# Kernel tuning notes

Hardware: AMD Instinct MI355X
Metric: run time of the kernel (lower is better)

## Reference

```python
import jax, jax.numpy as jnp
import numpy as np

B, S, D, H, L = 16, 1024, 128, 8, 3
DFF = 4 * D  # 512
DH = D // H  # 16
NUM_CLASSES = 6


def layernorm(x, g, b, eps):
    mu = jnp.mean(x, axis=-1, keepdims=True)
    var = jnp.mean(jnp.square(x - mu), axis=-1, keepdims=True)
    return g * (x - mu) / jnp.sqrt(var + eps) + b


def setup_inputs() -> dict:
    key = jax.random.key(0)
    ks = jax.random.split(key, 16)
    sc = 0.05
    inp = {
        'x': jax.random.normal(ks[0], (B, S, D), dtype=jnp.float32),
        'Wq': jax.random.normal(ks[1], (L, D, D), dtype=jnp.float32) * sc,
        'bq': jnp.zeros((L, D), dtype=jnp.float32),
        'Wk': jax.random.normal(ks[2], (L, D, D), dtype=jnp.float32) * sc,
        'bk': jnp.zeros((L, D), dtype=jnp.float32),
        'Wv': jax.random.normal(ks[3], (L, D, D), dtype=jnp.float32) * sc,
        'bv': jnp.zeros((L, D), dtype=jnp.float32),
        'ln1_g': jnp.ones((L, D), dtype=jnp.float32),
        'ln1_b': jnp.zeros((L, D), dtype=jnp.float32),
        'W1': jax.random.normal(ks[4], (L, D, DFF), dtype=jnp.float32) * sc,
        'b1': jnp.zeros((L, DFF), dtype=jnp.float32),
        'W2': jax.random.normal(ks[5], (L, DFF, D), dtype=jnp.float32) * sc,
        'b2': jnp.zeros((L, D), dtype=jnp.float32),
        'ln2_g': jnp.ones((L, D), dtype=jnp.float32),
        'ln2_b': jnp.zeros((L, D), dtype=jnp.float32),
        'Wout': jax.random.normal(ks[6], (D, NUM_CLASSES), dtype=jnp.float32) * sc,
        'bout': jnp.zeros((NUM_CLASSES,), dtype=jnp.float32),
    }
    return inp


def reference(x, Wq, bq, Wk, bk, Wv, bv, ln1_g, ln1_b, W1, b1, W2, b2, ln2_g, ln2_b, Wout, bout):
    scale = 1.0 / jnp.sqrt(jnp.float32(DH))
    for l in range(L):
        # Q/K/V projections with ReLU activation (as in source Dense(..., relu))
        q = jax.nn.relu(jnp.einsum('bsd,de->bse', x, Wq[l]) + bq[l])
        k = jax.nn.relu(jnp.einsum('bsd,de->bse', x, Wk[l]) + bk[l])
        v = jax.nn.relu(jnp.einsum('bsd,de->bse', x, Wv[l]) + bv[l])
        # split-heads (tf.split axis=-1 / concat axis=0 == reshape to heads)
        qh = q.reshape(B, S, H, DH)
        kh = k.reshape(B, S, H, DH)
        vh = v.reshape(B, S, H, DH)
        scores = jnp.einsum('bqhd,bkhd->bhqk', qh, kh) * scale  # [B,H,S,S]
        attn = jax.nn.softmax(scores, axis=-1)
        o = jnp.einsum('bhqk,bkhd->bqhd', attn, vh).reshape(B, S, D)
        x = layernorm(o + x, ln1_g[l], ln1_b[l], 1e-8)
        # pointwise FFN (Conv1D kernel_size=1 == dense over last dim)
        h = jax.nn.relu(jnp.einsum('bsd,df->bsf', x, W1[l]) + b1[l])
        f = jnp.einsum('bsf,fd->bsd', h, W2[l]) + b2[l]
        x = layernorm(f + x, ln2_g[l], ln2_b[l], 1e-6)
    return jnp.einsum('bsd,dc->bsc', x, Wout) + bout
```

## Files before the change

### kernel.cpp

```cpp
#include <hip/hip_runtime.h>
#include <math.h>

#define Bq 16
#define Sq 1024
#define Dq 128
#define Hq 8
#define DHq 16
#define DFFq 512
#define Lq 3
#define NCLS 6
#define NROWS (Bq * Sq)
#define NX ((size_t)NROWS * Dq)

#define QSCL 0.36067376022224085f

typedef __attribute__((ext_vector_type(8))) short    bf16x8;
typedef __attribute__((ext_vector_type(4))) float    f32x4;
typedef __attribute__((ext_vector_type(4))) _Float16 f16x4;
typedef __attribute__((ext_vector_type(8))) _Float16 f16x8;
typedef __attribute__((ext_vector_type(2))) _Float16 f16x2;

__device__ inline ushort f32_to_bf16(float f) {
    union { float f; unsigned u; } v; v.f = f;
    unsigned r = v.u + 0x7fffu + ((v.u >> 16) & 1u);
    return (ushort)(r >> 16);
}

__device__ __forceinline__ float exp2_raw(float x) {
    float r;
    asm("v_exp_f32 %0, %1" : "=v"(r) : "v"(x));
    return r;
}

__device__ __forceinline__ float rcp_fast(float x) {
    float r;
    asm("v_rcp_f32 %0, %1" : "=v"(r) : "v"(x));
    return r;
}

__device__ __forceinline__ f16x2 pkrtz(float a, float b) {
    return __builtin_bit_cast(f16x2, __builtin_amdgcn_cvt_pkrtz(a, b));
}

__global__ __launch_bounds__(256) void prep_kernel(
    const float* __restrict__ Wqp, const float* __restrict__ Wkp,
    const float* __restrict__ Wvp, const float* __restrict__ W1p,
    const float* __restrict__ W2p, const float* __restrict__ xp,
    ushort* __restrict__ wbf, ushort* __restrict__ xbf)
{
    const int gid = blockIdx.x * 256 + threadIdx.x;
    if (gid < 147456) {
        const int w   = gid / 49152;
        const int rem = gid - w * 49152;
        const int l   = rem >> 14;
        const int idx = rem & 16383;
        const int k   = idx >> 7;
        const int n   = idx & 127;
        const float* src = (w == 0) ? Wqp : (w == 1) ? Wkp : Wvp;
        const float scl = (w == 0) ? QSCL : 1.0f;
        wbf[(size_t)(w * 3 + l) * 16384 + n * 128 + k] =
            f32_to_bf16(src[(size_t)l * 16384 + k * 128 + n] * scl);
    } else if (gid < 344064) {
        const int g   = gid - 147456;
        const int l   = g >> 16;
        const int idx = g & 65535;
        const int k   = idx >> 9;
        const int n   = idx & 511;
        wbf[147456 + (size_t)l * 65536 + n * 128 + k] =
            f32_to_bf16(W1p[(size_t)l * 65536 + k * 512 + n]);
    } else if (gid < 540672) {
        const int g   = gid - 344064;
        const int l   = g >> 16;
        const int idx = g & 65535;
        const int k   = idx >> 7;
        const int n   = idx & 127;
        wbf[344064 + (size_t)l * 65536 + n * 512 + k] =
            f32_to_bf16(W2p[(size_t)l * 65536 + k * 128 + n]);
    } else {
        const int g = gid - 540672;
        xbf[g] = f32_to_bf16(xp[g]);
    }
}

__global__ __launch_bounds__(256) void gemm_qkv(
    const ushort* __restrict__ A,
    const ushort* __restrict__ wq, const ushort* __restrict__ wk,
    const ushort* __restrict__ wv,
    const float* __restrict__ bqp, const float* __restrict__ bkp,
    const float* __restrict__ bvp,
    _Float16* __restrict__ qo, _Float16* __restrict__ ko,
    _Float16* __restrict__ vo)
{
    __shared__ ushort As[64 * 40];
    __shared__ ushort Bs[128 * 40];

    const int sel  = blockIdx.y;
    const ushort* Bt   = (sel == 0) ? wq : (sel == 1) ? wk : wv;
    const float*  bias = (sel == 0) ? bqp : (sel == 1) ? bkp : bvp;
    const float   bscl = (sel == 0) ? QSCL : 1.0f;

    const int tid  = threadIdx.x;
    const int row0 = blockIdx.x * 64;
    const int wave = tid >> 6;
    const int lane = tid & 63;
    const int quad = lane >> 4;
    const int m16  = lane & 15;
    const int wm   = wave >> 1;
    const int wn   = wave & 1;

    const int sar = tid >> 2;
    const int sac = (tid & 3) * 8;

    f32x4 acc[2][4];
    #pragma unroll
    for (int i = 0; i < 2; ++i)
        #pragma unroll
        for (int j = 0; j < 4; ++j) acc[i][j] = (f32x4)0.f;

    const int r1 = tid >> 2, r2 = r1 + 64;

    bf16x8 av  = *(const bf16x8*)(A  + (size_t)(row0 + sar) * 128 + sac);
    bf16x8 bv1 = *(const bf16x8*)(Bt + (size_t)r1 * 128 + sac);
    bf16x8 bv2 = *(const bf16x8*)(Bt + (size_t)r2 * 128 + sac);

    for (int k0 = 0; k0 < 128; k0 += 32) {
        __syncthreads();
        *(bf16x8*)&As[sar * 40 + sac] = av;
        *(bf16x8*)&Bs[r1 * 40 + sac]  = bv1;
        *(bf16x8*)&Bs[r2 * 40 + sac]  = bv2;
        __syncthreads();

        if (k0 < 96) {
            av  = *(const bf16x8*)(A  + (size_t)(row0 + sar) * 128 + k0 + 32 + sac);
            bv1 = *(const bf16x8*)(Bt + (size_t)r1 * 128 + k0 + 32 + sac);
            bv2 = *(const bf16x8*)(Bt + (size_t)r2 * 128 + k0 + 32 + sac);
        }

        bf16x8 af[2], bf[4];
        #pragma unroll
        for (int i = 0; i < 2; ++i)
            af[i] = *(const bf16x8*)&As[(32 * wm + 16 * i + m16) * 40 + quad * 8];
        #pragma unroll
        for (int j = 0; j < 4; ++j)
            bf[j] = *(const bf16x8*)&Bs[(64 * wn + 16 * j + m16) * 40 + quad * 8];
        #pragma unroll
        for (int i = 0; i < 2; ++i)
            #pragma unroll
            for (int j = 0; j < 4; ++j)
                acc[i][j] = __builtin_amdgcn_mfma_f32_16x16x32_bf16(af[i], bf[j], acc[i][j], 0, 0, 0);
    }

    #pragma unroll
    for (int i = 0; i < 2; ++i) {
        #pragma unroll
        for (int j = 0; j < 4; ++j) {
            const int col = 64 * wn + 16 * j + m16;
            const float bb = bias[col] * bscl;
            const int hh = col >> 4, dh = col & 15;
            #pragma unroll
            for (int r = 0; r < 4; ++r) {
                float val = fmaxf(acc[i][j][r] + bb, 0.f);
                const int gr = row0 + 32 * wm + 16 * i + quad * 4 + r;
                const int b = gr >> 10, s = gr & 1023;
                if (sel == 2) {
                    vo[(((size_t)b * Hq + hh) * DHq + dh) * Sq + s] = (_Float16)val;
                } else {
                    _Float16* outp = (sel == 0) ? qo : ko;
                    outp[(((size_t)b * Hq + hh) * Sq + s) * DHq + dh] = (_Float16)val;
                }
            }
        }
    }
}

__global__ __launch_bounds__(256) void gemm_ffn_fused(
    const _Float16* __restrict__ o, const float* __restrict__ resid,
    const float* __restrict__ g1, const float* __restrict__ beta1,
    const ushort* __restrict__ W1t, const float* __restrict__ bias1,
    const ushort* __restrict__ W2t, const float* __restrict__ bias2,
    const float* __restrict__ g2, const float* __restrict__ beta2,
    float* __restrict__ xb,
    const ushort* __restrict__ wqn, const ushort* __restrict__ wkn,
    const ushort* __restrict__ wvn,
    const float* __restrict__ bqn, const float* __restrict__ bkn,
    const float* __restrict__ bvn,
    _Float16* __restrict__ qo, _Float16* __restrict__ ko,
    _Float16* __restrict__ vo, int do_next,
    const float* __restrict__ Wout, const float* __restrict__ bout,
    float* __restrict__ out, int last)
{
    __shared__ __align__(16) char smem[69120];
    ushort*    Af   = (ushort*)smem;
    ushort*    Hs   = (ushort*)(smem + 8704);
    ushort*    Bs   = (ushort*)(smem + 41984);
    float*     wo_s = (float*)(smem + 41984);
    _Float16*  vals = (_Float16*)(smem + 60416);
    float*     mus  = (float*)(smem + 68864);
    float*     rsds = (float*)(smem + 68992);

    const int tid  = threadIdx.x;
    const int row0 = blockIdx.x * 32;
    const int wave = tid >> 6;
    const int lane = tid & 63;
    const int quad = lane >> 4;
    const int m16  = lane & 15;
    const int wm   = wave >> 1;
    const int wn   = wave & 1;
    const int sac  = (tid & 3) * 8;
    const int r1   = tid >> 2, r2 = r1 + 64;

    const int ca = lane * 2;
    const float2 gg  = *(const float2*)(g1 + ca);
    const float2 bt1 = *(const float2*)(beta1 + ca);
    #pragma unroll 2
    for (int it = 0; it < 8; ++it) {
        const int rr = wave * 8 + it;
        const size_t base = (size_t)(row0 + rr) * Dq;
        const f16x2  ov = *(const f16x2*)(o + base + ca);
        const float2 rv = *(const float2*)(resid + base + ca);
        const float v0 = (float)ov[0] + rv.x;
        const float v1 = (float)ov[1] + rv.y;

        float s = v0 + v1;
        #pragma unroll
        for (int off = 32; off > 0; off >>= 1) s += __shfl_xor(s, off, 64);
        const float mu = s * (1.f / 128.f);
        const float d0 = v0 - mu, d1 = v1 - mu;
        float vs = d0 * d0 + d1 * d1;
        #pragma unroll
        for (int off = 32; off > 0; off >>= 1) vs += __shfl_xor(vs, off, 64);
        const float rstd = rsqrtf(vs * (1.f / 128.f) + 1e-8f);

        const float rv0 = gg.x * d0 * rstd + bt1.x;
        const float rv1 = gg.y * d1 * rstd + bt1.y;
        ushort2 ab; ab.x = f32_to_bf16(rv0); ab.y = f32_to_bf16(rv1);
        *(ushort2*)&Af[rr * 136 + ca] = ab;
        f16x2 vv; vv[0] = (_Float16)rv0; vv[1] = (_Float16)rv1;
        *(f16x2*)&vals[rr * 132 + ca] = vv;
    }

    f32x4 acc[4];
    #pragma unroll
    for (int j = 0; j < 4; ++j) acc[j] = (f32x4)0.f;

    bf16x8 w11 = *(const bf16x8*)(W1t + (size_t)r1 * 128 + sac);
    bf16x8 w12 = *(const bf16x8*)(W1t + (size_t)r1 * 128 + 32 + sac);
    bf16x8 w21 = *(const bf16x8*)(W1t + (size_t)r2 * 128 + sac);
    bf16x8 w22 = *(const bf16x8*)(W1t + (size_t)r2 * 128 + 32 + sac);

    for (int idx = 0; idx < 8; ++idx) {
        const int cc = idx >> 1;
        const int k0 = (idx & 1) * 64;

        __syncthreads();
        *(bf16x8*)&Bs[r1 * 72 + sac]      = w11;
        *(bf16x8*)&Bs[r1 * 72 + 32 + sac] = w12;
        *(bf16x8*)&Bs[r2 * 72 + sac]      = w21;
        *(bf16x8*)&Bs[r2 * 72 + 32 + sac] = w22;
        __syncthreads();

        if (idx < 7) {
            const int cc2 = (idx + 1) >> 1;
            const int k02 = ((idx + 1) & 1) * 64;
            w11 = *(const bf16x8*)(W1t + (size_t)(cc2 * 128 + r1) * 128 + k02 + sac);
            w12 = *(const bf16x8*)(W1t + (size_t)(cc2 * 128 + r1) * 128 + k02 + 32 + sac);
            w21 = *(const bf16x8*)(W1t + (size_t)(cc2 * 128 + r2) * 128 + k02 + sac);
            w22 = *(const bf16x8*)(W1t + (size_t)(cc2 * 128 + r2) * 128 + k02 + 32 + sac);
        }

        #pragma unroll
        for (int hh = 0; hh < 2; ++hh) {
            const int kk = k0 + hh * 32;
            const bf16x8 af = *(const bf16x8*)&Af[(16 * wm + m16) * 136 + kk + quad * 8];
            bf16x8 bf[4];
            #pragma unroll
            for (int j = 0; j < 4; ++j)
                bf[j] = *(const bf16x8*)&Bs[(64 * wn + 16 * j + m16) * 72 + hh * 32 + quad * 8];
            #pragma unroll
            for (int j = 0; j < 4; ++j)
                acc[j] = __builtin_amdgcn_mfma_f32_16x16x32_bf16(af, bf[j], acc[j], 0, 0, 0);
        }

        if (idx & 1) {
            #pragma unroll
            for (int j = 0; j < 4; ++j) {
                const int col = cc * 128 + 64 * wn + 16 * j + m16;
                const float bb = bias1[col];
                #pragma unroll
                for (int r = 0; r < 4; ++r) {
                    const int row = 16 * wm + quad * 4 + r;
                    Hs[row * 520 + col] = f32_to_bf16(fmaxf(acc[j][r] + bb, 0.f));
                }
                acc[j] = (f32x4)0.f;
            }
        }
    }

    f32x4 acc2[4];
    #pragma unroll
    for (int j = 0; j < 4; ++j) acc2[j] = (f32x4)0.f;

    w11 = *(const bf16x8*)(W2t + (size_t)r1 * DFFq + sac);
    w12 = *(const bf16x8*)(W2t + (size_t)r1 * DFFq + 32 + sac);
    w21 = *(const bf16x8*)(W2t + (size_t)r2 * DFFq + sac);
    w22 = *(const bf16x8*)(W2t + (size_t)r2 * DFFq + 32 + sac);

    for (int kc = 0; kc < 8; ++kc) {
        const int k0 = kc * 64;

        __syncthreads();
        *(bf16x8*)&Bs[r1 * 72 + sac]      = w11;
        *(bf16x8*)&Bs[r1 * 72 + 32 + sac] = w12;
        *(bf16x8*)&Bs[r2 * 72 + sac]      = w21;
        *(bf16x8*)&Bs[r2 * 72 + 32 + sac] = w22;
        __syncthreads();

        if (kc < 7) {
            const int k02 = (kc + 1) * 64;
            w11 = *(const bf16x8*)(W2t + (size_t)r1 * DFFq + k02 + sac);
            w12 = *(const bf16x8*)(W2t + (size_t)r1 * DFFq + k02 + 32 + sac);
            w21 = *(const bf16x8*)(W2t + (size_t)r2 * DFFq + k02 + sac);
            w22 = *(const bf16x8*)(W2t + (size_t)r2 * DFFq + k02 + 32 + sac);
        }

        #pragma unroll
        for (int hh = 0; hh < 2; ++hh) {
            const int kk = k0 + hh * 32;
            const bf16x8 af = *(const bf16x8*)&Hs[(16 * wm + m16) * 520 + kk + quad * 8];
            bf16x8 bf[4];
            #pragma unroll
            for (int j = 0; j < 4; ++j)
                bf[j] = *(const bf16x8*)&Bs[(64 * wn + 16 * j + m16) * 72 + hh * 32 + quad * 8];
            #pragma unroll
            for (int j = 0; j < 4; ++j)
                acc2[j] = __builtin_amdgcn_mfma_f32_16x16x32_bf16(af, bf[j], acc2[j], 0, 0, 0);
        }
    }

    __syncthreads();

    float vreg[4][4];
    #pragma unroll
    for (int j = 0; j < 4; ++j) {
        const int col = 64 * wn + 16 * j + m16;
        const float bb = bias2[col];
        #pragma unroll
        for (int r = 0; r < 4; ++r) {
            const int row = 16 * wm + quad * 4 + r;
            float v = acc2[j][r] + bb + (float)vals[row * 132 + col];
            vreg[j][r] = v;
            vals[row * 132 + col] = (_Float16)v;
        }
    }
    if (last) {
        #pragma unroll
        for (int i = 0; i < 3; ++i) wo_s[tid + i * 256] = Wout[tid + i * 256];
    }
    __syncthreads();

    {
        const int row = tid >> 3;
        const int c0  = (tid & 7) * 16;
        float s = 0.f, s2 = 0.f;
        #pragma unroll
        for (int u = 0; u < 4; ++u) {
            const f16x4 xv = *(const f16x4*)&vals[row * 132 + c0 + u * 4];
            #pragma unroll
            for (int e = 0; e < 4; ++e) {
                const float x = (float)xv[e];
                s += x; s2 = fmaf(x, x, s2);
            }
        }
        s  += __shfl_xor(s, 1, 64);  s  += __shfl_xor(s, 2, 64);  s  += __shfl_xor(s, 4, 64);
        s2 += __shfl_xor(s2, 1, 64); s2 += __shfl_xor(s2, 2, 64); s2 += __shfl_xor(s2, 4, 64);
        if ((tid & 7) == 0) {
            const float mu  = s * (1.f / 128.f);
            const float var = s2 * (1.f / 128.f) - mu * mu;
            mus[row]  = mu;
            rsds[row] = rsqrtf(var + 1e-6f);
        }
    }
    __syncthreads();

    if (!last) {
        #pragma unroll
        for (int j = 0; j < 4; ++j) {
            const int col = 64 * wn + 16 * j + m16;
            #pragma unroll
            for (int r = 0; r < 4; ++r) {
                const int row = 16 * wm + quad * 4 + r;
                const float rn = g2[col] * (vreg[j][r] - mus[row]) * rsds[row] + beta2[col];
                xb[(size_t)(row0 + row) * Dq + col] = rn;
                Af[row * 136 + col] = f32_to_bf16(rn);
            }
        }

        if (do_next) {
            bf16x8 q11 = *(const bf16x8*)(wqn + (size_t)r1 * 128 + sac);
            bf16x8 q12 = *(const bf16x8*)(wqn + (size_t)r1 * 128 + 32 + sac);
            bf16x8 q21 = *(const bf16x8*)(wqn + (size_t)r2 * 128 + sac);
            bf16x8 q22 = *(const bf16x8*)(wqn + (size_t)r2 * 128 + 32 + sac);

            f32x4 qacc[4];
            for (int st = 0; st < 6; ++st) {
                const int sel  = st >> 1;
                const int half = st & 1;
                if (half == 0) {
                    #pragma unroll
                    for (int j = 0; j < 4; ++j) qacc[j] = (f32x4)0.f;
                }

                __syncthreads();
                *(bf16x8*)&Bs[r1 * 72 + sac]      = q11;
                *(bf16x8*)&Bs[r1 * 72 + 32 + sac] = q12;
                *(bf16x8*)&Bs[r2 * 72 + sac]      = q21;
                *(bf16x8*)&Bs[r2 * 72 + 32 + sac] = q22;
                __syncthreads();

                if (st < 5) {
                    const int sel2 = (st + 1) >> 1;
                    const int k02  = ((st + 1) & 1) * 64;
                    const ushort* Bt2 = (sel2 == 0) ? wqn : (sel2 == 1) ? wkn : wvn;
                    q11 = *(const bf16x8*)(Bt2 + (size_t)r1 * 128 + k02 + sac);
                    q12 = *(const bf16x8*)(Bt2 + (size_t)r1 * 128 + k02 + 32 + sac);
                    q21 = *(const bf16x8*)(Bt2 + (size_t)r2 * 128 + k02 + sac);
                    q22 = *(const bf16x8*)(Bt2 + (size_t)r2 * 128 + k02 + 32 + sac);
                }

                const int k0 = half * 64;
                #pragma unroll
                for (int hh = 0; hh < 2; ++hh) {
                    const int kk = k0 + hh * 32;
                    const bf16x8 af = *(const bf16x8*)&Af[(16 * wm + m16) * 136 + kk + quad * 8];
                    bf16x8 bf[4];
                    #pragma unroll
                    for (int j = 0; j < 4; ++j)
                        bf[j] = *(const bf16x8*)&Bs[(64 * wn + 16 * j + m16) * 72 + hh * 32 + quad * 8];
                    #pragma unroll
                    for (int j = 0; j < 4; ++j)
                        qacc[j] = __builtin_amdgcn_mfma_f32_16x16x32_bf16(af, bf[j], qacc[j], 0, 0, 0);
                }

                if (half) {
                    const float* bias = (sel == 0) ? bqn : (sel == 1) ? bkn : bvn;
                    const float  bscl = (sel == 0) ? QSCL : 1.0f;
                    #pragma unroll
                    for (int j = 0; j < 4; ++j) {
                        const int col = 64 * wn + 16 * j + m16;
                        const float bb = bias[col] * bscl;
                        const int hh = col >> 4, dh = col & 15;
                        #pragma unroll
                        for (int r = 0; r < 4; ++r) {
                            float val = fmaxf(qacc[j][r] + bb, 0.f);
                            const int gr = row0 + 16 * wm + quad * 4 + r;
                            const int b = gr >> 10, s = gr & 1023;
                            if (sel == 2) {
                                vo[(((size_t)b * Hq + hh) * DHq + dh) * Sq + s] = (_Float16)val;
                            } else {
                                _Float16* outp = (sel == 0) ? qo : ko;
                                outp[(((size_t)b * Hq + hh) * Sq + s) * DHq + dh] = (_Float16)val;
                            }
                        }
                    }
                }
            }
        }
    } else {
        #pragma unroll
        for (int j = 0; j < 4; ++j) {
            const int col = 64 * wn + 16 * j + m16;
            #pragma unroll
            for (int r = 0; r < 4; ++r) {
                const int row = 16 * wm + quad * 4 + r;
                vals[row * 132 + col] =
                    (_Float16)(g2[col] * (vreg[j][r] - mus[row]) * rsds[row] + beta2[col]);
            }
        }
        __syncthreads();
        if (tid < 32 * NCLS) {
            const int row = tid / NCLS;
            const int c   = tid - row * NCLS;
            float a = bout[c];
            #pragma unroll 8
            for (int kk = 0; kk < Dq; ++kk)
                a = fmaf((float)vals[row * 132 + kk], wo_s[kk * NCLS + c], a);
            out[(size_t)(row0 + row) * NCLS + c] = a;
        }
    }
}

__global__ __launch_bounds__(256) void attn_mfma(
    const _Float16* __restrict__ q, const _Float16* __restrict__ k,
    const _Float16* __restrict__ vt, _Float16* __restrict__ o)
{
    __shared__ _Float16 Ks[256 * 20];
    __shared__ _Float16 Vs[16 * 264];

    const int bh   = blockIdx.x;
    const int qc   = blockIdx.y;
    const int b    = bh >> 3;
    const int h    = bh & 7;
    const int tid  = threadIdx.x;
    const int wave = tid >> 6;
    const int lane = tid & 63;
    const int quad = lane >> 4;
    const int m16  = lane & 15;
    const int q0   = qc * 128 + wave * 32;

    const f16x4 qf0 = *(const f16x4*)(q + (((size_t)bh * Sq) + q0 + m16) * DHq + quad * 4);
    const f16x4 qf1 = *(const f16x4*)(q + (((size_t)bh * Sq) + q0 + 16 + m16) * DHq + quad * 4);

    const _Float16* kg  = k  + (size_t)bh * Sq * DHq;
    const _Float16* vtg = vt + (size_t)bh * DHq * Sq;

    f32x4 oacc0 = (f32x4)0.f, oacc1 = (f32x4)0.f;
    f32x4 dacc0 = (f32x4)0.f, dacc1 = (f32x4)0.f;

    f16x4 onesf;
    onesf[0] = (_Float16)1.f; onesf[1] = (_Float16)1.f;
    onesf[2] = (_Float16)1.f; onesf[3] = (_Float16)1.f;

    const int krow = tid;
    const int vrow = tid >> 4;
    const int vcol = (tid & 15) * 16;

    f16x8 ka  = *(const f16x8*)(kg + (size_t)krow * DHq);
    f16x8 kb8 = *(const f16x8*)(kg + (size_t)krow * DHq + 8);
    f16x8 va  = *(const f16x8*)(vtg + (size_t)vrow * Sq + vcol);
    f16x8 vb  = *(const f16x8*)(vtg + (size_t)vrow * Sq + vcol + 8);

    for (int kb = 0; kb < 4; ++kb) {
        __syncthreads();
        *(f16x8*)&Ks[krow * 20 + 0] = ka;
        *(f16x8*)&Ks[krow * 20 + 8] = kb8;
        *(f16x8*)&Vs[vrow * 264 + vcol + 0] = va;
        *(f16x8*)&Vs[vrow * 264 + vcol + 8] = vb;
        __syncthreads();

        if (kb < 3) {
            const _Float16* kp = kg  + ((size_t)(kb + 1) * 256 + krow) * DHq;
            const _Float16* vp = vtg + (size_t)vrow * Sq + (kb + 1) * 256 + vcol;
            ka  = *(const f16x8*)(kp);
            kb8 = *(const f16x8*)(kp + 8);
            va  = *(const f16x8*)(vp);
            vb  = *(const f16x8*)(vp + 8);
        }

        __builtin_amdgcn_s_setprio(1);
        #pragma unroll 4
        for (int kt = 0; kt < 16; ++kt) {
            const f16x4 kf = *(const f16x4*)&Ks[(kt * 16 + m16) * 20 + quad * 4];
            const f16x4 vf = *(const f16x4*)&Vs[m16 * 264 + kt * 16 + quad * 4];

            f32x4 st0 = __builtin_amdgcn_mfma_f32_16x16x16f16(kf, qf0, (f32x4)0.f, 0, 0, 0);
            f32x4 st1 = __builtin_amdgcn_mfma_f32_16x16x16f16(kf, qf1, (f32x4)0.f, 0, 0, 0);

            const f16x2 a0 = pkrtz(exp2_raw(st0[0]), exp2_raw(st0[1]));
            const f16x2 a1 = pkrtz(exp2_raw(st0[2]), exp2_raw(st0[3]));
            const f16x2 b0 = pkrtz(exp2_raw(st1[0]), exp2_raw(st1[1]));
            const f16x2 b1 = pkrtz(exp2_raw(st1[2]), exp2_raw(st1[3]));

            const f16x4 pf0 = __builtin_shufflevector(a0, a1, 0, 1, 2, 3);
            const f16x4 pf1 = __builtin_shufflevector(b0, b1, 0, 1, 2, 3);

            oacc0 = __builtin_amdgcn_mfma_f32_16x16x16f16(pf0, vf, oacc0, 0, 0, 0);
            oacc1 = __builtin_amdgcn_mfma_f32_16x16x16f16(pf1, vf, oacc1, 0, 0, 0);
            dacc0 = __builtin_amdgcn_mfma_f32_16x16x16f16(pf0, onesf, dacc0, 0, 0, 0);
            dacc1 = __builtin_amdgcn_mfma_f32_16x16x16f16(pf1, onesf, dacc1, 0, 0, 0);
        }
        __builtin_amdgcn_s_setprio(0);
    }

    #pragma unroll
    for (int r = 0; r < 4; ++r) {
        const float i0 = rcp_fast(dacc0[r]);
        const float i1 = rcp_fast(dacc1[r]);
        o[((size_t)b * Sq + q0 + quad * 4 + r) * Dq + h * DHq + m16]      = (_Float16)(oacc0[r] * i0);
        o[((size_t)b * Sq + q0 + 16 + quad * 4 + r) * Dq + h * DHq + m16] = (_Float16)(oacc1[r] * i1);
    }
}

extern "C" void kernel_launch(void* const* d_in, const int* in_sizes, int n_in,
                              void* d_out, int out_size, void* d_ws, size_t ws_size,
                              hipStream_t stream)
{
    const float* x_in  = (const float*)d_in[0];
    const float* Wq    = (const float*)d_in[1];
    const float* bq    = (const float*)d_in[2];
    const float* Wk    = (const float*)d_in[3];
    const float* bk    = (const float*)d_in[4];
    const float* Wv    = (const float*)d_in[5];
    const float* bv    = (const float*)d_in[6];
    const float* ln1_g = (const float*)d_in[7];
    const float* ln1_b = (const float*)d_in[8];
    const float* W1    = (const float*)d_in[9];
    const float* b1    = (const float*)d_in[10];
    const float* W2    = (const float*)d_in[11];
    const float* b2    = (const float*)d_in[12];
    const float* ln2_g = (const float*)d_in[13];
    const float* ln2_b = (const float*)d_in[14];
    const float* Wout  = (const float*)d_in[15];
    const float* bout  = (const float*)d_in[16];
    float* out = (float*)d_out;

    float* ws = (float*)d_ws;
    _Float16* qf16 = (_Float16*)ws;
    _Float16* kf16 = (_Float16*)(ws + NX / 2);
    _Float16* vt16 = (_Float16*)(ws + NX);
    float*    xb   = ws + 9 * NX / 2;
    ushort*   xbf0 = (ushort*)(ws + 11 * NX / 2);
    ushort*   wbf  = (ushort*)(ws + 7 * NX);
    _Float16* obuf = (_Float16*)(ws + 8 * NX);

    prep_kernel<<<dim3(10304), dim3(256), 0, stream>>>(Wq, Wk, Wv, W1, W2, x_in, wbf, xbf0);

    const dim3 blk(256);

    {
        const ushort* wqt = wbf + (size_t)0 * 16384;
        const ushort* wkt = wbf + (size_t)3 * 16384;
        const ushort* wvt = wbf + (size_t)6 * 16384;
        gemm_qkv<<<dim3(256, 3), blk, 0, stream>>>(
            xbf0, wqt, wkt, wvt, bq, bk, bv, qf16, kf16, vt16);
    }

    const float* xcur = x_in;
    for (int l = 0; l < Lq; ++l) {
        const ushort* w1t = wbf + 147456 + (size_t)l * 65536;
        const ushort* w2t = wbf + 344064 + (size_t)l * 65536;
        const int next = (l < Lq - 1) ? 1 : 0;
        const int ln   = l + 1;
        const ushort* wqn = next ? (wbf + (size_t)(0 * 3 + ln) * 16384) : wbf;
        const ushort* wkn = next ? (wbf + (size_t)(1 * 3 + ln) * 16384) : wbf;
        const ushort* wvn = next ? (wbf + (size_t)(2 * 3 + ln) * 16384) : wbf;
        const float*  bqn = next ? (bq + ln * Dq) : bq;
        const float*  bkn = next ? (bk + ln * Dq) : bk;
        const float*  bvn = next ? (bv + ln * Dq) : bv;

        attn_mfma<<<dim3(Bq * Hq, 8), blk, 0, stream>>>(qf16, kf16, vt16, obuf);

        gemm_ffn_fused<<<dim3(512), blk, 0, stream>>>(
            obuf, xcur, ln1_g + l * Dq, ln1_b + l * Dq,
            w1t, b1 + l * DFFq, w2t, b2 + l * Dq,
            ln2_g + l * Dq, ln2_b + l * Dq,
            xb,
            wqn, wkn, wvn, bqn, bkn, bvn,
            qf16, kf16, vt16, next,
            Wout, bout, out, (l == Lq - 1) ? 1 : 0);

        xcur = xb;
    }
}
```

Measured before the change: 244.3 us.

## Interleave FFN1/FFN2 per 128-column chunk to shrink LDS and raise occupancy

Restructures the fused FFN kernel so each 128-wide chunk of the hidden layer is computed and immediately consumed by the second GEMM, replacing the full 32x512 hidden buffer with a 32x128 chunk buffer. This cuts shared memory from about 69KB to about 44.5KB, and a launch-bounds hint asks for three blocks per CU. It also batches the residual/attention loads before the LayerNorm loop, and prefetches the next layer's Wq tile in the last FFN step. The cost is more accumulator registers live at once (acc and acc2) under a tighter register budget, which risks spills.

```diff
diff --git a/kernel.cpp b/kernel.cpp
--- a/kernel.cpp
+++ b/kernel.cpp
@@ -173,7 +173,7 @@
     }
 }
 
-__global__ __launch_bounds__(256) void gemm_ffn_fused(
+__global__ __launch_bounds__(256, 3) void gemm_ffn_fused(
     const _Float16* __restrict__ o, const float* __restrict__ resid,
     const float* __restrict__ g1, const float* __restrict__ beta1,
     const ushort* __restrict__ W1t, const float* __restrict__ bias1,
@@ -189,14 +189,14 @@
     const float* __restrict__ Wout, const float* __restrict__ bout,
     float* __restrict__ out, int last)
 {
-    __shared__ __align__(16) char smem[69120];
+    __shared__ __align__(16) char smem[44544];
     ushort*    Af   = (ushort*)smem;
-    ushort*    Hs   = (ushort*)(smem + 8704);
-    ushort*    Bs   = (ushort*)(smem + 41984);
-    float*     wo_s = (float*)(smem + 41984);
-    _Float16*  vals = (_Float16*)(smem + 60416);
-    float*     mus  = (float*)(smem + 68864);
-    float*     rsds = (float*)(smem + 68992);
+    ushort*    Hcc  = (ushort*)(smem + 8704);
+    ushort*    Bs   = (ushort*)(smem + 17408);
+    float*     wo_s = (float*)(smem + 17408);
+    _Float16*  vals = (_Float16*)(smem + 35840);
+    float*     mus  = (float*)(smem + 44288);
+    float*     rsds = (float*)(smem + 44416);
 
     const int tid  = threadIdx.x;
     const int row0 = blockIdx.x * 32;
@@ -212,14 +212,19 @@
     const int ca = lane * 2;
     const float2 gg  = *(const float2*)(g1 + ca);
     const float2 bt1 = *(const float2*)(beta1 + ca);
-    #pragma unroll 2
+    f16x2  ovv[8];
+    float2 rvv[8];
+    #pragma unroll
+    for (int it = 0; it < 8; ++it) {
+        const size_t base = (size_t)(row0 + wave * 8 + it) * Dq;
+        ovv[it] = *(const f16x2*)(o + base + ca);
+        rvv[it] = *(const float2*)(resid + base + ca);
+    }
+    #pragma unroll
     for (int it = 0; it < 8; ++it) {
         const int rr = wave * 8 + it;
-        const size_t base = (size_t)(row0 + rr) * Dq;
-        const f16x2  ov = *(const f16x2*)(o + base + ca);
-        const float2 rv = *(const float2*)(resid + base + ca);
-        const float v0 = (float)ov[0] + rv.x;
-        const float v1 = (float)ov[1] + rv.y;
+        const float v0 = (float)ovv[it][0] + rvv[it].x;
+        const float v1 = (float)ovv[it][1] + rvv[it].y;
 
         float s = v0 + v1;
         #pragma unroll
@@ -239,18 +244,20 @@
         *(f16x2*)&vals[rr * 132 + ca] = vv;
     }
 
-    f32x4 acc[4];
-    #pragma unroll
-    for (int j = 0; j < 4; ++j) acc[j] = (f32x4)0.f;
+    f32x4 acc[4], acc2[4];
+    #pragma unroll
+    for (int j = 0; j < 4; ++j) { acc[j] = (f32x4)0.f; acc2[j] = (f32x4)0.f; }
 
     bf16x8 w11 = *(const bf16x8*)(W1t + (size_t)r1 * 128 + sac);
     bf16x8 w12 = *(const bf16x8*)(W1t + (size_t)r1 * 128 + 32 + sac);
     bf16x8 w21 = *(const bf16x8*)(W1t + (size_t)r2 * 128 + sac);
     bf16x8 w22 = *(const bf16x8*)(W1t + (size_t)r2 * 128 + 32 + sac);
 
-    for (int idx = 0; idx < 8; ++idx) {
-        const int cc = idx >> 1;
-        const int k0 = (idx & 1) * 64;
+    #pragma unroll
+    for (int t = 0; t < 16; ++t) {
+        const int cc   = t >> 2;
+        const int ph   = (t >> 1) & 1;
+        const int half = t & 1;
 
         __syncthreads();
         *(bf16x8*)&Bs[r1 * 72 + sac]      = w11;
@@ -259,81 +266,61 @@
         *(bf16x8*)&Bs[r2 * 72 + 32 + sac] = w22;
         __syncthreads();
 
-        if (idx < 7) {
-            const int cc2 = (idx + 1) >> 1;
-            const int k02 = ((idx + 1) & 1) * 64;
-            w11 = *(const bf16x8*)(W1t + (size_t)(cc2 * 128 + r1) * 128 + k02 + sac);
-            w12 = *(const bf16x8*)(W1t + (size_t)(cc2 * 128 + r1) * 128 + k02 + 32 + sac);
-            w21 = *(const bf16x8*)(W1t + (size_t)(cc2 * 128 + r2) * 128 + k02 + sac);
-            w22 = *(const bf16x8*)(W1t + (size_t)(cc2 * 128 + r2) * 128 + k02 + 32 + sac);
-        }
-
+        if (t < 15) {
+            const int tn  = t + 1;
+            const int nc  = tn >> 2, np = (tn >> 1) & 1, nh = tn & 1;
+            if (np == 0) {
+                const ushort* p = W1t + (size_t)(nc * 128) * 128 + nh * 64;
+                w11 = *(const bf16x8*)(p + (size_t)r1 * 128 + sac);
+                w12 = *(const bf16x8*)(p + (size_t)r1 * 128 + 32 + sac);
+                w21 = *(const bf16x8*)(p + (size_t)r2 * 128 + sac);
+                w22 = *(const bf16x8*)(p + (size_t)r2 * 128 + 32 + sac);
+            } else {
+                const ushort* p = W2t + nc * 128 + nh * 64;
+                w11 = *(const bf16x8*)(p + (size_t)r1 * 512 + sac);
+                w12 = *(const bf16x8*)(p + (size_t)r1 * 512 + 32 + sac);
+                w21 = *(const bf16x8*)(p + (size_t)r2 * 512 + sac);
+                w22 = *(const bf16x8*)(p + (size_t)r2 * 512 + 32 + sac);
+            }
+        } else if (do_next) {
+            w11 = *(const bf16x8*)(wqn + (size_t)r1 * 128 + sac);
+            w12 = *(const bf16x8*)(wqn + (size_t)r1 * 128 + 32 + sac);
+            w21 = *(const bf16x8*)(wqn + (size_t)r2 * 128 + sac);
+            w22 = *(const bf16x8*)(wqn + (size_t)r2 * 128 + 32 + sac);
+        }
+
+        const ushort* Asrc = ph ? Hcc : Af;
         #pragma unroll
         for (int hh = 0; hh < 2; ++hh) {
-            const int kk = k0 + hh * 32;
-            const bf16x8 af = *(const bf16x8*)&Af[(16 * wm + m16) * 136 + kk + quad * 8];
+            const int kk = half * 64 + hh * 32;
+            const bf16x8 af = *(const bf16x8*)&Asrc[(16 * wm + m16) * 136 + kk + quad * 8];
             bf16x8 bf[4];
             #pragma unroll
             for (int j = 0; j < 4; ++j)
                 bf[j] = *(const bf16x8*)&Bs[(64 * wn + 16 * j + m16) * 72 + hh * 32 + quad * 8];
-            #pragma unroll
-            for (int j = 0; j < 4; ++j)
-                acc[j] = __builtin_amdgcn_mfma_f32_16x16x32_bf16(af, bf[j], acc[j], 0, 0, 0);
-        }
-
-        if (idx & 1) {
+            if (ph == 0) {
+                #pragma unroll
+                for (int j = 0; j < 4; ++j)
+                    acc[j] = __builtin_amdgcn_mfma_f32_16x16x32_bf16(af, bf[j], acc[j], 0, 0, 0);
+            } else {
+                #pragma unroll
+                for (int j = 0; j < 4; ++j)
+                    acc2[j] = __builtin_amdgcn_mfma_f32_16x16x32_bf16(af, bf[j], acc2[j], 0, 0, 0);
+            }
+        }
+
+        if (ph == 0 && half == 1) {
             #pragma unroll
             for (int j = 0; j < 4; ++j) {
-                const int col = cc * 128 + 64 * wn + 16 * j + m16;
-                const float bb = bias1[col];
+                const int col_l = 64 * wn + 16 * j + m16;
+                const float bb = bias1[cc * 128 + col_l];
                 #pragma unroll
                 for (int r = 0; r < 4; ++r) {
                     const int row = 16 * wm + quad * 4 + r;
-                    Hs[row * 520 + col] = f32_to_bf16(fmaxf(acc[j][r] + bb, 0.f));
+                    Hcc[row * 136 + col_l] = f32_to_bf16(fmaxf(acc[j][r] + bb, 0.f));
                 }
                 acc[j] = (f32x4)0.f;
             }
-        }
-    }
-
-    f32x4 acc2[4];
-    #pragma unroll
-    for (int j = 0; j < 4; ++j) acc2[j] = (f32x4)0.f;
-
-    w11 = *(const bf16x8*)(W2t + (size_t)r1 * DFFq + sac);
-    w12 = *(const bf16x8*)(W2t + (size_t)r1 * DFFq + 32 + sac);
-    w21 = *(const bf16x8*)(W2t + (size_t)r2 * DFFq + sac);
-    w22 = *(const bf16x8*)(W2t + (size_t)r2 * DFFq + 32 + sac);
-
-    for (int kc = 0; kc < 8; ++kc) {
-        const int k0 = kc * 64;
-
-        __syncthreads();
-        *(bf16x8*)&Bs[r1 * 72 + sac]      = w11;
-        *(bf16x8*)&Bs[r1 * 72 + 32 + sac] = w12;
-        *(bf16x8*)&Bs[r2 * 72 + sac]      = w21;
-        *(bf16x8*)&Bs[r2 * 72 + 32 + sac] = w22;
-        __syncthreads();
-
-        if (kc < 7) {
-            const int k02 = (kc + 1) * 64;
-            w11 = *(const bf16x8*)(W2t + (size_t)r1 * DFFq + k02 + sac);
-            w12 = *(const bf16x8*)(W2t + (size_t)r1 * DFFq + k02 + 32 + sac);
-            w21 = *(const bf16x8*)(W2t + (size_t)r2 * DFFq + k02 + sac);
-            w22 = *(const bf16x8*)(W2t + (size_t)r2 * DFFq + k02 + 32 + sac);
-        }
-
-        #pragma unroll
-        for (int hh = 0; hh < 2; ++hh) {
-            const int kk = k0 + hh * 32;
-            const bf16x8 af = *(const bf16x8*)&Hs[(16 * wm + m16) * 520 + kk + quad * 8];
-            bf16x8 bf[4];
-            #pragma unroll
-            for (int j = 0; j < 4; ++j)
-                bf[j] = *(const bf16x8*)&Bs[(64 * wn + 16 * j + m16) * 72 + hh * 32 + quad * 8];
-            #pragma unroll
-            for (int j = 0; j < 4; ++j)
-                acc2[j] = __builtin_amdgcn_mfma_f32_16x16x32_bf16(af, bf[j], acc2[j], 0, 0, 0);
         }
     }
 
@@ -396,12 +383,8 @@
         }
 
         if (do_next) {
-            bf16x8 q11 = *(const bf16x8*)(wqn + (size_t)r1 * 128 + sac);
-            bf16x8 q12 = *(const bf16x8*)(wqn + (size_t)r1 * 128 + 32 + sac);
-            bf16x8 q21 = *(const bf16x8*)(wqn + (size_t)r2 * 128 + sac);
-            bf16x8 q22 = *(const bf16x8*)(wqn + (size_t)r2 * 128 + 32 + sac);
-
             f32x4 qacc[4];
+            #pragma unroll
             for (int st = 0; st < 6; ++st) {
                 const int sel  = st >> 1;
                 const int half = st & 1;
@@ -411,20 +394,20 @@
                 }
 
                 __syncthreads();
-                *(bf16x8*)&Bs[r1 * 72 + sac]      = q11;
-                *(bf16x8*)&Bs[r1 * 72 + 32 + sac] = q12;
-                *(bf16x8*)&Bs[r2 * 72 + sac]      = q21;
-                *(bf16x8*)&Bs[r2 * 72 + 32 + sac] = q22;
+                *(bf16x8*)&Bs[r1 * 72 + sac]      = w11;
+                *(bf16x8*)&Bs[r1 * 72 + 32 + sac] = w12;
+                *(bf16x8*)&Bs[r2 * 72 + sac]      = w21;
+                *(bf16x8*)&Bs[r2 * 72 + 32 + sac] = w22;
                 __syncthreads();
 
                 if (st < 5) {
                     const int sel2 = (st + 1) >> 1;
                     const int k02  = ((st + 1) & 1) * 64;
                     const ushort* Bt2 = (sel2 == 0) ? wqn : (sel2 == 1) ? wkn : wvn;
-                    q11 = *(const bf16x8*)(Bt2 + (size_t)r1 * 128 + k02 + sac);
-                    q12 = *(const bf16x8*)(Bt2 + (size_t)r1 * 128 + k02 + 32 + sac);
-                    q21 = *(const bf16x8*)(Bt2 + (size_t)r2 * 128 + k02 + sac);
-                    q22 = *(const bf16x8*)(Bt2 + (size_t)r2 * 128 + k02 + 32 + sac);
+                    w11 = *(const bf16x8*)(Bt2 + (size_t)r1 * 128 + k02 + sac);
+                    w12 = *(const bf16x8*)(Bt2 + (size_t)r1 * 128 + k02 + 32 + sac);
+                    w21 = *(const bf16x8*)(Bt2 + (size_t)r2 * 128 + k02 + sac);
+                    w22 = *(const bf16x8*)(Bt2 + (size_t)r2 * 128 + k02 + 32 + sac);
                 }
 
                 const int k0 = half * 64;
```

New measurement: 240.7 us. Within noise of the previous version (-1.4%).
